# Optimization experiments

Hardware: AMD Instinct MI355X
Metric: run time of the kernel (lower is better)

The kernel has to match this reference:

```python
import jax, jax.numpy as jnp
import numpy as np

DECAY = 0.99
EPS = 1e-05


def setup_inputs() -> dict:
    key = jax.random.key(0)
    k1, k2 = jax.random.split(key)
    B, C, H, W = 16, 64, 32, 32
    K = 8192
    z_e = jax.random.normal(k1, (B, C, H, W), dtype=jnp.float32)
    embedding = jax.random.normal(k2, (K, C), dtype=jnp.float32)
    cluster_size = jnp.zeros((K,), dtype=jnp.float32)
    embedding_avg = embedding  # initialized as a clone of the codebook
    return {"z_e": z_e, "embedding": embedding, "cluster_size": cluster_size,
            "embedding_avg": embedding_avg}


def reference(z_e, embedding, cluster_size, embedding_avg):
    B, C, H, W = z_e.shape
    K = embedding.shape[0]
    # [N, C] tokens
    z_flat = jnp.transpose(z_e, (0, 2, 3, 1)).reshape(-1, C)
    d = ((z_flat * z_flat).sum(-1, keepdims=True)
         - 2.0 * (z_flat @ embedding.T)
         + (embedding * embedding).sum(-1))
    indices = jnp.argmin(d, axis=1)  # [N] int
    z_q_flat = embedding[indices]    # [N, C]
    z_q = jnp.transpose(z_q_flat.reshape(B, H, W, C), (0, 3, 1, 2))
    # EMA codebook update (training path); one-hot matmuls expressed as segment sums
    counts = jax.ops.segment_sum(jnp.ones(z_flat.shape[0], dtype=z_flat.dtype),
                                 indices, num_segments=K)            # encodings.sum(0)
    dw = jax.ops.segment_sum(z_flat, indices, num_segments=K)        # encodings.T @ z_flat
    new_cluster_size = DECAY * cluster_size + (1.0 - DECAY) * counts
    new_embedding_avg = DECAY * embedding_avg + (1.0 - DECAY) * dw
    n = new_cluster_size.sum()
    cs = (new_cluster_size + EPS) / (n + K * EPS) * n
    new_embedding = new_embedding_avg / cs[:, None]
    # straight-through estimator
    z_q_st = z_e + jax.lax.stop_gradient(z_q - z_e)
    return (z_q_st, indices.reshape(B, H * W), z_q,
            new_embedding, new_cluster_size, new_embedding_avg)
```

## Files before the change

kernel.cpp:

```cpp
#include <hip/hip_runtime.h>

#define DECAYF 0.99f
#define OMDF   0.01f
#define TAU    3.5e-2f

typedef unsigned int u32;
typedef unsigned long long u64;
typedef __attribute__((ext_vector_type(8))) _Float16 f16x8;
typedef __attribute__((ext_vector_type(4))) float f32x4;

#define EN_OFF     0
#define EFRAG_OFF  32768
#define IDX_OFF    32768
#define BEST1_OFF  2129920
#define BEST2_OFF  4227072
#define CNT_OFF    5275648

__device__ __forceinline__ u64 enc_pair(float s, int idx) {
  u32 u = __float_as_uint(s);
  u = (u & 0x80000000u) ? ~u : (u | 0x80000000u);
  return ((u64)u << 32) | (u32)(~idx);
}
__device__ __forceinline__ float dec_score(u64 e) {
  u32 u = (u32)(e >> 32);
  u = (u & 0x80000000u) ? (u & 0x7fffffffu) : ~u;
  return __uint_as_float(u);
}
__device__ __forceinline__ int dec_idx(u64 e) { return (int)(~(u32)e); }
__device__ __forceinline__ unsigned short f2h(float f) {
  union { _Float16 h; unsigned short u; } v;
  v.h = (_Float16)f;
  return v.u;
}
__device__ __forceinline__ float exact_dot(const float* __restrict__ sx,
                                           const float* __restrict__ emb, int k) {
  const float4* e = (const float4*)(emb + (size_t)k * 64);
  float a = 0.f;
#pragma unroll
  for (int q = 0; q < 16; ++q) {
    float4 v = e[q];
    a = fmaf(sx[4 * q],     v.x, a);
    a = fmaf(sx[4 * q + 1], v.y, a);
    a = fmaf(sx[4 * q + 2], v.z, a);
    a = fmaf(sx[4 * q + 3], v.w, a);
  }
  return a;
}

__global__ __launch_bounds__(256) void k_prep(const float* __restrict__ emb,
                                              const float* __restrict__ cs_in,
                                              const float* __restrict__ avg_in,
                                              const float* __restrict__ z_e,
                                              float* __restrict__ en,
                                              unsigned char* __restrict__ efrag,
                                              unsigned char* __restrict__ zfrag,
                                              float* __restrict__ out4,
                                              float* __restrict__ out5,
                                              float* __restrict__ nsum) {
  __shared__ float warr[4];
  __shared__ float sx[64][129];
  int bid = blockIdx.x;
  int t = threadIdx.x;
  if (bid < 512) {
    int tid = bid * 256 + t;
    int k = tid >> 4, q = tid & 15;
    float4 v = ((const float4*)emb)[tid];
    ushort4 hv;
    hv.x = f2h(v.x); hv.y = f2h(v.y); hv.z = f2h(v.z); hv.w = f2h(v.w);
    size_t off = (size_t)(k >> 4) * 2048 + (size_t)(q >> 3) * 1024
               + (size_t)((q >> 1) & 3) * 256 + (size_t)(k & 15) * 16
               + (size_t)(q & 1) * 8;
    *(ushort4*)(efrag + off) = hv;
    float s = v.x * v.x + v.y * v.y + v.z * v.z + v.w * v.w;
    s += __shfl_xor(s, 1, 16);
    s += __shfl_xor(s, 2, 16);
    s += __shfl_xor(s, 4, 16);
    s += __shfl_xor(s, 8, 16);
    if (q == 0) en[k] = 0.5f * s;
  } else if (bid < 1031) {
    int tid = (bid - 512) * 256 + t;
    if (tid < 131072) {
      float4 v = ((const float4*)avg_in)[tid];
      v.x *= DECAYF; v.y *= DECAYF; v.z *= DECAYF; v.w *= DECAYF;
      ((float4*)out5)[tid] = v;
    }
  } else if (bid == 1031) {
    float s = 0.f;
#pragma unroll
    for (int q = 0; q < 8; ++q) {
      int idx = q * 256 + t;
      float4 v = ((const float4*)cs_in)[idx];
      v.x *= DECAYF; v.y *= DECAYF; v.z *= DECAYF; v.w *= DECAYF;
      ((float4*)out4)[idx] = v;
      s += v.x + v.y + v.z + v.w;
    }
    s += __shfl_xor(s, 1, 64);
    s += __shfl_xor(s, 2, 64);
    s += __shfl_xor(s, 4, 64);
    s += __shfl_xor(s, 8, 64);
    s += __shfl_xor(s, 16, 64);
    s += __shfl_xor(s, 32, 64);
    if ((t & 63) == 0) warr[t >> 6] = s;
    __syncthreads();
    if (t == 0) *nsum = warr[0] + warr[1] + warr[2] + warr[3];
  } else {
    int n0 = (bid - 1032) * 128;
    int b = n0 >> 10, hwb = n0 & 1023;
#pragma unroll
    for (int r = 0; r < 8; ++r) {
      int g = r * 256 + t;
      int c = g >> 5, f4 = g & 31;
      float4 v = *(const float4*)(z_e + ((size_t)b << 16) + ((size_t)c << 10)
                                  + hwb + f4 * 4);
      sx[c][f4 * 4 + 0] = v.x;
      sx[c][f4 * 4 + 1] = v.y;
      sx[c][f4 * 4 + 2] = v.z;
      sx[c][f4 * 4 + 3] = v.w;
    }
    __syncthreads();
#pragma unroll
    for (int r = 0; r < 4; ++r) {
      int id = r * 256 + t;
      int nl = id & 127, k = id >> 7;
      int n = n0 + nl;
      unsigned short u[8];
#pragma unroll
      for (int j = 0; j < 8; ++j) u[j] = f2h(sx[k * 8 + j][nl]);
      size_t off = (size_t)(n >> 4) * 2048 + (size_t)(k >> 2) * 1024
                 + (size_t)(k & 3) * 256 + (size_t)(n & 15) * 16;
      *(ushort4*)(zfrag + off)     = make_ushort4(u[0], u[1], u[2], u[3]);
      *(ushort4*)(zfrag + off + 8) = make_ushort4(u[4], u[5], u[6], u[7]);
    }
  }
}

__global__ __launch_bounds__(256) void k_argmin_mfma(
    const unsigned char* __restrict__ zfrag,
    const unsigned char* __restrict__ efrag,
    const float* __restrict__ en, u64* __restrict__ best1,
    float* __restrict__ best2) {
  __shared__ float sen[512];
  const int sl = blockIdx.x & 15;
  const int wave = threadIdx.x >> 6, lane = threadIdx.x & 63;
  const int tg = (blockIdx.x >> 4) * 4 + wave;
  const int col = lane & 15, g4 = lane >> 4;
  const int scb = sl << 9;

  if (threadIdx.x < 128)
    ((float4*)sen)[threadIdx.x] = ((const float4*)(en + scb))[threadIdx.x];
  __syncthreads();

  f16x8 a[4][2];
  {
    const unsigned char* zb = zfrag + (size_t)(tg * 4) * 2048
                            + (size_t)g4 * 256 + (size_t)col * 16;
#pragma unroll
    for (int tt = 0; tt < 4; ++tt) {
      a[tt][0] = *(const f16x8*)(zb + tt * 2048);
      a[tt][1] = *(const f16x8*)(zb + tt * 2048 + 1024);
    }
  }
  float b1[16], b2[16];
#pragma unroll
  for (int r = 0; r < 16; ++r) { b1[r] = -3.0e38f; b2[r] = -3.0e38f; }

  const unsigned char* gb = efrag + (size_t)scb * 128 + (size_t)lane * 16;

  auto body = [&](int t, f16x8 u0, f16x8 u1) {
    const float negen = -sen[t * 16 + col];
    f32x4 acc0, acc1, acc2, acc3;
#pragma unroll
    for (int r = 0; r < 4; ++r) { acc0[r] = negen; acc1[r] = negen;
                                  acc2[r] = negen; acc3[r] = negen; }
    acc0 = __builtin_amdgcn_mfma_f32_16x16x32_f16(a[0][0], u0, acc0, 0, 0, 0);
    acc1 = __builtin_amdgcn_mfma_f32_16x16x32_f16(a[1][0], u0, acc1, 0, 0, 0);
    acc2 = __builtin_amdgcn_mfma_f32_16x16x32_f16(a[2][0], u0, acc2, 0, 0, 0);
    acc3 = __builtin_amdgcn_mfma_f32_16x16x32_f16(a[3][0], u0, acc3, 0, 0, 0);
    acc0 = __builtin_amdgcn_mfma_f32_16x16x32_f16(a[0][1], u1, acc0, 0, 0, 0);
    acc1 = __builtin_amdgcn_mfma_f32_16x16x32_f16(a[1][1], u1, acc1, 0, 0, 0);
    acc2 = __builtin_amdgcn_mfma_f32_16x16x32_f16(a[2][1], u1, acc2, 0, 0, 0);
    acc3 = __builtin_amdgcn_mfma_f32_16x16x32_f16(a[3][1], u1, acc3, 0, 0, 0);
    const u32 emb6 = (u32)(63 - t);
#pragma unroll
    for (int r = 0; r < 4; ++r) {
      float f0 = __uint_as_float((__float_as_uint(acc0[r]) & 0xFFFFFFC0u) | emb6);
      b2[r] = __builtin_amdgcn_fmed3f(f0, b1[r], b2[r]);
      b1[r] = fmaxf(b1[r], f0);
      float f1 = __uint_as_float((__float_as_uint(acc1[r]) & 0xFFFFFFC0u) | emb6);
      b2[4 + r] = __builtin_amdgcn_fmed3f(f1, b1[4 + r], b2[4 + r]);
      b1[4 + r] = fmaxf(b1[4 + r], f1);
      float f2 = __uint_as_float((__float_as_uint(acc2[r]) & 0xFFFFFFC0u) | emb6);
      b2[8 + r] = __builtin_amdgcn_fmed3f(f2, b1[8 + r], b2[8 + r]);
      b1[8 + r] = fmaxf(b1[8 + r], f2);
      float f3 = __uint_as_float((__float_as_uint(acc3[r]) & 0xFFFFFFC0u) | emb6);
      b2[12 + r] = __builtin_amdgcn_fmed3f(f3, b1[12 + r], b2[12 + r]);
      b1[12 + r] = fmaxf(b1[12 + r], f3);
    }
  };

  f16x8 c0 = *(const f16x8*)(gb);
  f16x8 c1 = *(const f16x8*)(gb + 1024);
  f16x8 d0 = *(const f16x8*)(gb + 2048);
  f16x8 d1 = *(const f16x8*)(gb + 3072);
  for (int t = 0; t < 32; t += 2) {
    f16x8 u0 = c0, u1 = c1;
    if (t + 2 < 32) {
      c0 = *(const f16x8*)(gb + (size_t)(t + 2) * 2048);
      c1 = *(const f16x8*)(gb + (size_t)(t + 2) * 2048 + 1024);
    }
    body(t, u0, u1);
    u0 = d0; u1 = d1;
    if (t + 3 < 32) {
      d0 = *(const f16x8*)(gb + (size_t)(t + 3) * 2048);
      d1 = *(const f16x8*)(gb + (size_t)(t + 3) * 2048 + 1024);
    }
    body(t + 1, u0, u1);
  }

  int mi[16];
#pragma unroll
  for (int r = 0; r < 16; ++r) mi[r] = col;
#pragma unroll
  for (int st = 1; st < 16; st <<= 1) {
#pragma unroll
    for (int r = 0; r < 16; ++r) {
      float ob1 = __shfl_xor(b1[r], st, 64);
      float ob2 = __shfl_xor(b2[r], st, 64);
      int omi = __shfl_xor(mi[r], st, 64);
      bool ogt = ob1 > b1[r];
      b2[r] = fmaxf(fminf(b1[r], ob1), fmaxf(b2[r], ob2));
      mi[r] = ogt ? omi : mi[r];
      b1[r] = fmaxf(b1[r], ob1);
    }
  }
  if (col == 0) {
#pragma unroll
    for (int r = 0; r < 16; ++r) {
      int tt = r >> 2, rr = r & 3;
      int token = tg * 64 + tt * 16 + g4 * 4 + rr;
      int t = 63 - (int)(__float_as_uint(b1[r]) & 63u);
      int gcode = scb + t * 16 + mi[r];
      best1[(size_t)sl * 16384 + token] = enc_pair(b1[r], gcode);
      best2[(size_t)sl * 16384 + token] = b2[r];
    }
  }
}

__global__ __launch_bounds__(256) void k_resfix(const float* __restrict__ z_e,
                                                const float* __restrict__ emb,
                                                const float* __restrict__ en,
                                                const u64* __restrict__ best1,
                                                const float* __restrict__ best2,
                                                int* __restrict__ idxa) {
  __shared__ float sxr[64];
  __shared__ int flist[64];
  __shared__ float fth[64];
  __shared__ int nflag;
  __shared__ u32 fmask;
  __shared__ u64 red;
  int t = threadIdx.x;
  int n0 = blockIdx.x * 64;
  if (t == 0) nflag = 0;
  __syncthreads();
  if (t < 64) {
    int n = n0 + t;
    u64 e[16];
#pragma unroll
    for (int s = 0; s < 16; ++s) e[s] = best1[(size_t)s * 16384 + n];
    u64 top = e[0];
#pragma unroll
    for (int s = 1; s < 16; ++s) top = e[s] > top ? e[s] : top;
    float second = -3.0e38f;
#pragma unroll
    for (int s = 0; s < 16; ++s)
      second = fmaxf(second, best2[(size_t)s * 16384 + n]);
#pragma unroll
    for (int s = 0; s < 16; ++s)
      if (e[s] != top) second = fmaxf(second, dec_score(e[s]));
    idxa[n] = dec_idx(top);
    if (dec_score(top) - second < TAU) {
      int p = atomicAdd(&nflag, 1);
      flist[p] = n;
      fth[p] = dec_score(top);
    }
  }
  __syncthreads();
  int nf = nflag;
  for (int i = 0; i < nf; ++i) {
    int n = flist[i];
    float theta = fth[i] - TAU;
    if (t == 0) { fmask = 0; red = 0ull; }
    if (t < 64) {
      sxr[t] = z_e[((size_t)(n >> 10) << 16) + ((size_t)t << 10) + (n & 1023)];
    }
    __syncthreads();
    u64 myb = 0ull;
    if (t < 16) {
      u64 es = best1[(size_t)t * 16384 + n];
      if (best2[(size_t)t * 16384 + n] >= theta) atomicOr(&fmask, 1u << t);
      if (dec_score(es) >= theta) {
        int k = dec_idx(es);
        float a = exact_dot(sxr, emb, k) - en[k];
        myb = enc_pair(a, k);
      }
    }
    __syncthreads();
    u32 fm = fmask;
    while (fm) {
      int s = __ffs(fm) - 1;
      fm &= fm - 1;
      int k0 = (s << 9) + t;
      float a0 = exact_dot(sxr, emb, k0)       - en[k0];
      float a1 = exact_dot(sxr, emb, k0 + 256) - en[k0 + 256];
      u64 m0 = enc_pair(a0, k0), m1 = enc_pair(a1, k0 + 256);
      u64 mm = m0 > m1 ? m0 : m1;
      myb = mm > myb ? mm : myb;
    }
    if (myb) atomicMax(&red, myb);
    __syncthreads();
    if (t == 0) idxa[n] = dec_idx(red);
    __syncthreads();
  }
}

__global__ __launch_bounds__(256) void k_scatter(const float* __restrict__ z_e,
                                                 const int* __restrict__ idxa,
                                                 float* __restrict__ out4,
                                                 float* __restrict__ out5) {
  int tid = blockIdx.x * 256 + threadIdx.x;
  int n = tid >> 6, c = tid & 63;
  int idx = idxa[n];
  int b = n >> 10, hw = n & 1023;
  float x = z_e[((size_t)b << 16) + ((size_t)c << 10) + hw];
  atomicAdd(out5 + (size_t)idx * 64 + c, OMDF * x);
  if (c == 0) atomicAdd(out4 + idx, OMDF);
}

__global__ __launch_bounds__(256) void k_gather(const float* __restrict__ z_e,
                                                const float* __restrict__ emb,
                                                const int* __restrict__ idxa,
                                                float* __restrict__ out0,
                                                float* __restrict__ out1,
                                                float* __restrict__ out2) {
  int tid = blockIdx.x * 256 + threadIdx.x;
  int hw4 = tid & 255;
  int c   = (tid >> 8) & 63;
  int b   = tid >> 14;
  int n0  = (b << 10) + (hw4 << 2);
  size_t off = ((size_t)b << 16) + ((size_t)c << 10) + ((size_t)hw4 << 2);
  float4 z = *(const float4*)(z_e + off);
  int i0 = idxa[n0], i1 = idxa[n0 + 1], i2 = idxa[n0 + 2], i3 = idxa[n0 + 3];
  float4 q;
  q.x = emb[(size_t)i0 * 64 + c];
  q.y = emb[(size_t)i1 * 64 + c];
  q.z = emb[(size_t)i2 * 64 + c];
  q.w = emb[(size_t)i3 * 64 + c];
  float4 st;
  st.x = z.x + (q.x - z.x);
  st.y = z.y + (q.y - z.y);
  st.z = z.z + (q.z - z.z);
  st.w = z.w + (q.w - z.w);
  *(float4*)(out2 + off) = q;
  *(float4*)(out0 + off) = st;
  if (c == 0) {
    float4 f = make_float4((float)i0, (float)i1, (float)i2, (float)i3);
    *(float4*)(out1 + n0) = f;
  }
}

__global__ __launch_bounds__(256) void k_final(const float* __restrict__ out4,
                                               const float* __restrict__ out5,
                                               const float* __restrict__ nsum,
                                               float* __restrict__ out3) {
  int tid = blockIdx.x * 256 + threadIdx.x;
  int k = tid >> 4;
  double nn  = (double)*nsum + 163.84;
  double ncs = (double)out4[k];
  double cs  = (ncs + 1e-5) / (nn + 8192.0 * 1e-5) * nn;
  float inv  = (float)(1.0 / cs);
  float4 v = ((const float4*)out5)[tid];
  v.x *= inv; v.y *= inv; v.z *= inv; v.w *= inv;
  ((float4*)out3)[tid] = v;
}

extern "C" void kernel_launch(void* const* d_in, const int* in_sizes, int n_in,
                              void* d_out, int out_size, void* d_ws, size_t ws_size,
                              hipStream_t stream) {
  const float* z_e    = (const float*)d_in[0];
  const float* emb    = (const float*)d_in[1];
  const float* cs_in  = (const float*)d_in[2];
  const float* avg_in = (const float*)d_in[3];

  float* out  = (float*)d_out;
  float* out0 = out;
  float* out1 = out0 + 1048576;
  float* out2 = out1 + 16384;
  float* out3 = out2 + 1048576;
  float* out4 = out3 + 524288;
  float* out5 = out4 + 8192;

  char* ws = (char*)d_ws;
  float* en            = (float*)(ws + EN_OFF);
  unsigned char* efrag = (unsigned char*)(ws + EFRAG_OFF);
  u64* best1           = (u64*)(ws + BEST1_OFF);
  float* best2         = (float*)(ws + BEST2_OFF);
  int* idxa            = (int*)(ws + IDX_OFF);
  float* nsum          = (float*)(ws + CNT_OFF + 4);
  unsigned char* zfrag = (unsigned char*)out0;

  k_prep       <<<1160, 256, 0, stream>>>(emb, cs_in, avg_in, z_e, en, efrag,
                                          zfrag, out4, out5, nsum);
  k_argmin_mfma<<<1024, 256, 0, stream>>>(zfrag, efrag, en, best1, best2);
  k_resfix     <<<256,  256, 0, stream>>>(z_e, emb, en, best1, best2, idxa);
  k_scatter    <<<4096, 256, 0, stream>>>(z_e, idxa, out4, out5);
  k_gather     <<<1024, 256, 0, stream>>>(z_e, emb, idxa, out0, out1, out2);
  k_final      <<<512,  256, 0, stream>>>(out4, out5, nsum, out3);
}
```

Before: 147.3 us.

## Halve per-wave token tile in argmin kernel and fuse scatter into gather

```diff
diff --git a/kernel.cpp b/kernel.cpp
--- a/kernel.cpp
+++ b/kernel.cpp
@@ -150,36 +150,30 @@
     ((float4*)sen)[threadIdx.x] = ((const float4*)(en + scb))[threadIdx.x];
   __syncthreads();
 
-  f16x8 a[4][2];
+  f16x8 a[2][2];
   {
-    const unsigned char* zb = zfrag + (size_t)(tg * 4) * 2048
+    const unsigned char* zb = zfrag + (size_t)(tg * 2) * 2048
                             + (size_t)g4 * 256 + (size_t)col * 16;
-#pragma unroll
-    for (int tt = 0; tt < 4; ++tt) {
-      a[tt][0] = *(const f16x8*)(zb + tt * 2048);
-      a[tt][1] = *(const f16x8*)(zb + tt * 2048 + 1024);
-    }
-  }
-  float b1[16], b2[16];
-#pragma unroll
-  for (int r = 0; r < 16; ++r) { b1[r] = -3.0e38f; b2[r] = -3.0e38f; }
+    a[0][0] = *(const f16x8*)(zb);
+    a[0][1] = *(const f16x8*)(zb + 1024);
+    a[1][0] = *(const f16x8*)(zb + 2048);
+    a[1][1] = *(const f16x8*)(zb + 3072);
+  }
+  float b1[8], b2[8];
+#pragma unroll
+  for (int r = 0; r < 8; ++r) { b1[r] = -3.0e38f; b2[r] = -3.0e38f; }
 
   const unsigned char* gb = efrag + (size_t)scb * 128 + (size_t)lane * 16;
 
   auto body = [&](int t, f16x8 u0, f16x8 u1) {
     const float negen = -sen[t * 16 + col];
-    f32x4 acc0, acc1, acc2, acc3;
-#pragma unroll
-    for (int r = 0; r < 4; ++r) { acc0[r] = negen; acc1[r] = negen;
-                                  acc2[r] = negen; acc3[r] = negen; }
+    f32x4 acc0, acc1;
+#pragma unroll
+    for (int r = 0; r < 4; ++r) { acc0[r] = negen; acc1[r] = negen; }
     acc0 = __builtin_amdgcn_mfma_f32_16x16x32_f16(a[0][0], u0, acc0, 0, 0, 0);
     acc1 = __builtin_amdgcn_mfma_f32_16x16x32_f16(a[1][0], u0, acc1, 0, 0, 0);
-    acc2 = __builtin_amdgcn_mfma_f32_16x16x32_f16(a[2][0], u0, acc2, 0, 0, 0);
-    acc3 = __builtin_amdgcn_mfma_f32_16x16x32_f16(a[3][0], u0, acc3, 0, 0, 0);
     acc0 = __builtin_amdgcn_mfma_f32_16x16x32_f16(a[0][1], u1, acc0, 0, 0, 0);
     acc1 = __builtin_amdgcn_mfma_f32_16x16x32_f16(a[1][1], u1, acc1, 0, 0, 0);
-    acc2 = __builtin_amdgcn_mfma_f32_16x16x32_f16(a[2][1], u1, acc2, 0, 0, 0);
-    acc3 = __builtin_amdgcn_mfma_f32_16x16x32_f16(a[3][1], u1, acc3, 0, 0, 0);
     const u32 emb6 = (u32)(63 - t);
 #pragma unroll
     for (int r = 0; r < 4; ++r) {
@@ -189,12 +183,6 @@
       float f1 = __uint_as_float((__float_as_uint(acc1[r]) & 0xFFFFFFC0u) | emb6);
       b2[4 + r] = __builtin_amdgcn_fmed3f(f1, b1[4 + r], b2[4 + r]);
       b1[4 + r] = fmaxf(b1[4 + r], f1);
-      float f2 = __uint_as_float((__float_as_uint(acc2[r]) & 0xFFFFFFC0u) | emb6);
-      b2[8 + r] = __builtin_amdgcn_fmed3f(f2, b1[8 + r], b2[8 + r]);
-      b1[8 + r] = fmaxf(b1[8 + r], f2);
-      float f3 = __uint_as_float((__float_as_uint(acc3[r]) & 0xFFFFFFC0u) | emb6);
-      b2[12 + r] = __builtin_amdgcn_fmed3f(f3, b1[12 + r], b2[12 + r]);
-      b1[12 + r] = fmaxf(b1[12 + r], f3);
     }
   };
 
@@ -217,13 +205,13 @@
     body(t + 1, u0, u1);
   }
 
-  int mi[16];
-#pragma unroll
-  for (int r = 0; r < 16; ++r) mi[r] = col;
+  int mi[8];
+#pragma unroll
+  for (int r = 0; r < 8; ++r) mi[r] = col;
 #pragma unroll
   for (int st = 1; st < 16; st <<= 1) {
 #pragma unroll
-    for (int r = 0; r < 16; ++r) {
+    for (int r = 0; r < 8; ++r) {
       float ob1 = __shfl_xor(b1[r], st, 64);
       float ob2 = __shfl_xor(b2[r], st, 64);
       int omi = __shfl_xor(mi[r], st, 64);
@@ -235,9 +223,9 @@
   }
   if (col == 0) {
 #pragma unroll
-    for (int r = 0; r < 16; ++r) {
+    for (int r = 0; r < 8; ++r) {
       int tt = r >> 2, rr = r & 3;
-      int token = tg * 64 + tt * 16 + g4 * 4 + rr;
+      int token = tg * 32 + tt * 16 + g4 * 4 + rr;
       int t = 63 - (int)(__float_as_uint(b1[r]) & 63u);
       int gcode = scb + t * 16 + mi[r];
       best1[(size_t)sl * 16384 + token] = enc_pair(b1[r], gcode);
@@ -323,48 +311,52 @@
   }
 }
 
-__global__ __launch_bounds__(256) void k_scatter(const float* __restrict__ z_e,
-                                                 const int* __restrict__ idxa,
-                                                 float* __restrict__ out4,
-                                                 float* __restrict__ out5) {
-  int tid = blockIdx.x * 256 + threadIdx.x;
-  int n = tid >> 6, c = tid & 63;
-  int idx = idxa[n];
-  int b = n >> 10, hw = n & 1023;
-  float x = z_e[((size_t)b << 16) + ((size_t)c << 10) + hw];
-  atomicAdd(out5 + (size_t)idx * 64 + c, OMDF * x);
-  if (c == 0) atomicAdd(out4 + idx, OMDF);
-}
-
 __global__ __launch_bounds__(256) void k_gather(const float* __restrict__ z_e,
                                                 const float* __restrict__ emb,
                                                 const int* __restrict__ idxa,
                                                 float* __restrict__ out0,
                                                 float* __restrict__ out1,
-                                                float* __restrict__ out2) {
+                                                float* __restrict__ out2,
+                                                float* __restrict__ out4,
+                                                float* __restrict__ out5) {
   int tid = blockIdx.x * 256 + threadIdx.x;
-  int hw4 = tid & 255;
-  int c   = (tid >> 8) & 63;
-  int b   = tid >> 14;
-  int n0  = (b << 10) + (hw4 << 2);
-  size_t off = ((size_t)b << 16) + ((size_t)c << 10) + ((size_t)hw4 << 2);
-  float4 z = *(const float4*)(z_e + off);
-  int i0 = idxa[n0], i1 = idxa[n0 + 1], i2 = idxa[n0 + 2], i3 = idxa[n0 + 3];
-  float4 q;
-  q.x = emb[(size_t)i0 * 64 + c];
-  q.y = emb[(size_t)i1 * 64 + c];
-  q.z = emb[(size_t)i2 * 64 + c];
-  q.w = emb[(size_t)i3 * 64 + c];
-  float4 st;
-  st.x = z.x + (q.x - z.x);
-  st.y = z.y + (q.y - z.y);
-  st.z = z.z + (q.z - z.z);
-  st.w = z.w + (q.w - z.w);
-  *(float4*)(out2 + off) = q;
-  *(float4*)(out0 + off) = st;
-  if (c == 0) {
-    float4 f = make_float4((float)i0, (float)i1, (float)i2, (float)i3);
-    *(float4*)(out1 + n0) = f;
+  {
+    int hw4 = tid & 255;
+    int c   = (tid >> 8) & 63;
+    int b   = tid >> 14;
+    int n0  = (b << 10) + (hw4 << 2);
+    size_t off = ((size_t)b << 16) + ((size_t)c << 10) + ((size_t)hw4 << 2);
+    float4 z = *(const float4*)(z_e + off);
+    int i0 = idxa[n0], i1 = idxa[n0 + 1], i2 = idxa[n0 + 2], i3 = idxa[n0 + 3];
+    float4 q;
+    q.x = emb[(size_t)i0 * 64 + c];
+    q.y = emb[(size_t)i1 * 64 + c];
+    q.z = emb[(size_t)i2 * 64 + c];
+    q.w = emb[(size_t)i3 * 64 + c];
+    float4 st;
+    st.x = z.x + (q.x - z.x);
+    st.y = z.y + (q.y - z.y);
+    st.z = z.z + (q.z - z.z);
+    st.w = z.w + (q.w - z.w);
+    *(float4*)(out2 + off) = q;
+    *(float4*)(out0 + off) = st;
+    if (c == 0) {
+      float4 f = make_float4((float)i0, (float)i1, (float)i2, (float)i3);
+      *(float4*)(out1 + n0) = f;
+    }
+  }
+  {
+    int c = tid & 63;
+    int nb = (tid >> 6) * 4;
+#pragma unroll
+    for (int i = 0; i < 4; ++i) {
+      int n = nb + i;
+      int idx = idxa[n];
+      int b = n >> 10, hw = n & 1023;
+      float x = z_e[((size_t)b << 16) + ((size_t)c << 10) + hw];
+      atomicAdd(out5 + (size_t)idx * 64 + c, OMDF * x);
+      if (c == 0) atomicAdd(out4 + idx, OMDF);
+    }
   }
 }
 
@@ -410,9 +402,9 @@
 
   k_prep       <<<1160, 256, 0, stream>>>(emb, cs_in, avg_in, z_e, en, efrag,
                                           zfrag, out4, out5, nsum);
-  k_argmin_mfma<<<1024, 256, 0, stream>>>(zfrag, efrag, en, best1, best2);
+  k_argmin_mfma<<<2048, 256, 0, stream>>>(zfrag, efrag, en, best1, best2);
   k_resfix     <<<256,  256, 0, stream>>>(z_e, emb, en, best1, best2, idxa);
-  k_scatter    <<<4096, 256, 0, stream>>>(z_e, idxa, out4, out5);
-  k_gather     <<<1024, 256, 0, stream>>>(z_e, emb, idxa, out0, out1, out2);
+  k_gather     <<<1024, 256, 0, stream>>>(z_e, emb, idxa, out0, out1, out2,
+                                          out4, out5);
   k_final      <<<512,  256, 0, stream>>>(out4, out5, nsum, out3);
 }
```

After: 145.9 us. No clear change (-1.0%).
